# Optimization experiments

Hardware: AMD Instinct MI355X
Metric: run time of the kernel (lower is better)

## Reference

```python
import jax, jax.numpy as jnp
import numpy as np

B, N, DIM = 4, 2048, 1024
HEADS, DIM_HEAD = 16, 64
HIDDEN = HEADS * DIM_HEAD  # 1024
SCALE = 1.0 / np.sqrt(DIM_HEAD).astype(np.float32)


def setup_inputs() -> dict:
    key = jax.random.key(0)
    k1, k2, k3 = jax.random.split(key, 3)
    x = jax.random.normal(k1, (B, N, DIM), dtype=jnp.float32)
    # Linear(dim, 3*hidden, bias=False): stored as [in, out] for x @ W
    w_qkv = jax.random.normal(k2, (DIM, 3 * HIDDEN), dtype=jnp.float32) * (1.0 / np.sqrt(DIM))
    w_out = jax.random.normal(k3, (HIDDEN, DIM), dtype=jnp.float32) * (1.0 / np.sqrt(HIDDEN))
    b_out = jnp.zeros((DIM,), dtype=jnp.float32)
    return {"x": x, "w_qkv": w_qkv, "w_out": w_out, "b_out": b_out}


def reference(x, w_qkv, w_out, b_out):
    b, n, _ = x.shape
    qkv = x @ w_qkv                                  # [b, n, 3*hidden]
    q, k, v = jnp.split(qkv, 3, axis=-1)             # each [b, n, hidden]

    def to_heads(t):
        return t.reshape(b, n, HEADS, DIM_HEAD).transpose(0, 2, 1, 3)  # [b, h, n, d]

    q, k, v = to_heads(q), to_heads(k), to_heads(v)
    scores = jnp.einsum('bhid,bhjd->bhij', q, k) * SCALE   # [b, h, n_q, n_k]
    # Faithful to original: softmax over dim=2 (the QUERY axis), not keys.
    attn = jax.nn.softmax(scores, axis=2)
    y = jnp.einsum('bhij,bhjd->bhid', attn, v)             # [b, h, n, d]
    y = y.transpose(0, 2, 1, 3).reshape(b, n, HIDDEN)      # [b, n, hidden]
    return y @ w_out + b_out
```

## Files before the change

kernel.cpp:

```cpp
#include <hip/hip_runtime.h>
#include <math.h>
#include <stdint.h>

#define B_    4
#define N_    2048
#define DIM_  1024
#define H_    16
#define DH_   64
#define HID_  1024
#define RS_   3072
#define C2_   0.1803368801111204f

typedef unsigned short u16;
typedef unsigned int   u32;
typedef short  bf16x8 __attribute__((ext_vector_type(8)));
typedef u16    u16x8  __attribute__((ext_vector_type(8)));
typedef float  f32x4  __attribute__((ext_vector_type(4)));
typedef float  f32x16 __attribute__((ext_vector_type(16)));
typedef unsigned int u32x2 __attribute__((ext_vector_type(2)));

__device__ inline u16 f2b(float x) {
    u32 u = __float_as_uint(x);
    return (u16)((u + 0x7fffu + ((u >> 16) & 1u)) >> 16);
}
__device__ inline float b2f(u16 x) {
    return __uint_as_float((u32)x << 16);
}

__device__ inline u32 pack2bf(float f0, float f1) {
    u32 u0 = __float_as_uint(f0) + 0x8000u;
    u32 u1 = __float_as_uint(f1) + 0x8000u;
    return __builtin_amdgcn_perm(u1, u0, 0x07060302u);
}

__device__ inline void pl32swap(u32 &a, u32 &b) {
#if __has_builtin(__builtin_amdgcn_permlane32_swap)
    u32x2 r = __builtin_amdgcn_permlane32_swap(a, b, false, false);
    a = r[0]; b = r[1];
#else
    asm("v_permlane32_swap_b32 %0, %1" : "+v"(a), "+v"(b));
#endif
}

#if defined(__has_builtin)
#if __has_builtin(__builtin_amdgcn_global_load_lds)
#define USE_GLL 1
#endif
#endif

#ifdef USE_GLL
typedef const __attribute__((address_space(1))) u32* gas_ptr;
typedef __attribute__((address_space(3))) u32* las_ptr;
__device__ inline void gll16(const void* g, void* l) {
    __builtin_amdgcn_global_load_lds((gas_ptr)g, (las_ptr)l, 16, 0, 0);
}
#endif

__global__ __launch_bounds__(256) void cast_bf16(const float* __restrict__ in,
                                                 u16* __restrict__ out, int n) {
    int i = (blockIdx.x * 256 + threadIdx.x) * 8;
    if (i >= n) return;
    float4 a = *(const float4*)&in[i];
    float4 b = *(const float4*)&in[i + 4];
    u16x8 p;
    p[0] = f2b(a.x); p[1] = f2b(a.y); p[2] = f2b(a.z); p[3] = f2b(a.w);
    p[4] = f2b(b.x); p[5] = f2b(b.y); p[6] = f2b(b.z); p[7] = f2b(b.w);
    *(u16x8*)&out[i] = p;
}

__global__ __launch_bounds__(256) void transpose_cast(const float* __restrict__ W,
                                                      u16* __restrict__ Wt,
                                                      int K, int Nn, int qcols) {
    __shared__ float t[64][65];
    const int tid = threadIdx.x;
    const int k0 = blockIdx.y * 64, n0 = blockIdx.x * 64;
    for (int idx = tid; idx < 64 * 16; idx += 256) {
        int r = idx >> 4, c4 = (idx & 15) * 4;
        float4 g = *(const float4*)&W[(size_t)(k0 + r) * Nn + n0 + c4];
        t[r][c4] = g.x; t[r][c4 + 1] = g.y; t[r][c4 + 2] = g.z; t[r][c4 + 3] = g.w;
    }
    __syncthreads();
    for (int idx = tid; idx < 64 * 8; idx += 256) {
        int n = idx >> 3, k8 = (idx & 7) * 8;
        float s = (n0 + n < qcols) ? C2_ : 1.0f;
        u16x8 p;
        #pragma unroll
        for (int u = 0; u < 8; u++) p[u] = f2b(t[k8 + u][n] * s);
        *(u16x8*)&Wt[(size_t)(n0 + n) * K + k0 + k8] = p;
    }
}

template<int BF16OUT>
__global__ __launch_bounds__(256) void gemm_bt(const u16* __restrict__ A,
                                               const u16* __restrict__ Bt,
                                               const float* __restrict__ bias,
                                               void* __restrict__ Cout,
                                               int M, int Nn, int K) {
    __shared__ u16 at[128 * 32];
    __shared__ u16 bt[128 * 32];
    const int tid = threadIdx.x;
    const int lane = tid & 63, wave = tid >> 6;
    const int wr = wave >> 1, wc = wave & 1;
    const int mlane = lane & 15, quad = lane >> 4;
    const int id = blockIdx.x;
    const int mt = (id & 7) * 8 + ((id >> 3) & 7);
    const int nt = id >> 6;
    const int m0 = mt * 128, n0 = nt * 128;
    const int r = tid >> 2, kc = (tid & 3) * 8;

    f32x4 acc[4][4] = {};

    for (int k0 = 0; k0 < K; k0 += 32) {
        __syncthreads();
#ifdef USE_GLL
        gll16(&A[(size_t)(m0 + r) * K + k0 + kc],       &at[r * 32 + kc]);
        gll16(&A[(size_t)(m0 + r + 64) * K + k0 + kc],  &at[(r + 64) * 32 + kc]);
        gll16(&Bt[(size_t)(n0 + r) * K + k0 + kc],      &bt[r * 32 + kc]);
        gll16(&Bt[(size_t)(n0 + r + 64) * K + k0 + kc], &bt[(r + 64) * 32 + kc]);
#else
        *(u16x8*)&at[r * 32 + kc]        = *(const u16x8*)&A[(size_t)(m0 + r) * K + k0 + kc];
        *(u16x8*)&at[(r + 64) * 32 + kc] = *(const u16x8*)&A[(size_t)(m0 + r + 64) * K + k0 + kc];
        *(u16x8*)&bt[r * 32 + kc]        = *(const u16x8*)&Bt[(size_t)(n0 + r) * K + k0 + kc];
        *(u16x8*)&bt[(r + 64) * 32 + kc] = *(const u16x8*)&Bt[(size_t)(n0 + r + 64) * K + k0 + kc];
#endif
        __syncthreads();

        bf16x8 af[4], bf[4];
        #pragma unroll
        for (int rt = 0; rt < 4; rt++)
            af[rt] = *(const bf16x8*)&at[(wr * 64 + rt * 16 + mlane) * 32 + quad * 8];
        #pragma unroll
        for (int ct = 0; ct < 4; ct++)
            bf[ct] = *(const bf16x8*)&bt[(wc * 64 + ct * 16 + mlane) * 32 + quad * 8];
        #pragma unroll
        for (int rt = 0; rt < 4; rt++)
            #pragma unroll
            for (int ct = 0; ct < 4; ct++)
                acc[rt][ct] = __builtin_amdgcn_mfma_f32_16x16x32_bf16(af[rt], bf[ct], acc[rt][ct], 0, 0, 0);
    }

    const int row0 = m0 + wr * 64 + quad * 4;
    const int col0 = n0 + wc * 64 + mlane;
    #pragma unroll
    for (int rt = 0; rt < 4; rt++)
        #pragma unroll
        for (int ct = 0; ct < 4; ct++) {
            int c = col0 + ct * 16;
            float bv = (!BF16OUT && bias != nullptr) ? bias[c] : 0.f;
            #pragma unroll
            for (int reg = 0; reg < 4; reg++) {
                int rr = row0 + rt * 16 + reg;
                float v = acc[rt][ct][reg] + bv;
                if (BF16OUT) ((u16*)Cout)[(size_t)rr * Nn + c] = f2b(v);
                else         ((float*)Cout)[(size_t)rr * Nn + c] = v;
            }
        }
}

__global__ __launch_bounds__(256) void attn_stats_vt(const u16* __restrict__ qkvb,
                                                     u16* __restrict__ vT) {
    __shared__ u16 kt[64 * 72];
    __shared__ u16 qt[4][64 * 72];
    __shared__ float red[4][64];
    __shared__ float li[64];

    const int tid = threadIdx.x;
    const int lane = tid & 63, wave = tid >> 6;
    const int mlane = lane & 15, quad = lane >> 4;
    const int id = blockIdx.x;
    const int bh = (id & 7) * 8 + ((id >> 3) & 7);
    const int b = bh >> 4, h = bh & 15;
    const int j0 = (id >> 6) * 64;

    const u16* qbase = qkvb + (size_t)b * N_ * RS_ + h * DH_;
    const u16* kbase = qbase + HID_;
    const u16* vbase = qbase + 2 * HID_;

    for (int idx = tid; idx < 512; idx += 256) {
        int r = idx >> 3, d8 = (idx & 7) * 8;
        *(u16x8*)&kt[r * 72 + d8] = *(const u16x8*)&kbase[(size_t)(j0 + r) * RS_ + d8];
    }
    __syncthreads();

    bf16x8 kf[4][2];
    #pragma unroll
    for (int t = 0; t < 4; t++)
        #pragma unroll
        for (int ks = 0; ks < 2; ks++)
            kf[t][ks] = *(const bf16x8*)&kt[(t * 16 + mlane) * 72 + ks * 32 + quad * 8];

    f32x4 acc[4] = {};
    u16* qw = &qt[wave][0];

    const int prr = lane >> 3, pd8 = (lane & 7) * 8;
    u16x8 pq[8];
    #pragma unroll
    for (int t = 0; t < 8; t++)
        pq[t] = *(const u16x8*)&qbase[(size_t)(wave * 64 + t * 8 + prr) * RS_ + pd8];

    for (int i0 = wave * 64; i0 < N_; i0 += 256) {
        #pragma unroll
        for (int t = 0; t < 8; t++)
            *(u16x8*)&qw[(t * 8 + prr) * 72 + pd8] = pq[t];
        int in = i0 + 256;
        if (in < N_) {
            #pragma unroll
            for (int t = 0; t < 8; t++)
                pq[t] = *(const u16x8*)&qbase[(size_t)(in + t * 8 + prr) * RS_ + pd8];
        }
        #pragma unroll
        for (int q4 = 0; q4 < 4; q4++) {
            bf16x8 bq0 = *(const bf16x8*)&qw[(q4 * 16 + mlane) * 72 + quad * 8];
            bf16x8 bq1 = *(const bf16x8*)&qw[(q4 * 16 + mlane) * 72 + 32 + quad * 8];
            #pragma unroll
            for (int t = 0; t < 4; t++) {
                f32x4 z = {0.f, 0.f, 0.f, 0.f};
                z = __builtin_amdgcn_mfma_f32_16x16x32_bf16(kf[t][0], bq0, z, 0, 0, 0);
                z = __builtin_amdgcn_mfma_f32_16x16x32_bf16(kf[t][1], bq1, z, 0, 0, 0);
                #pragma unroll
                for (int reg = 0; reg < 4; reg++)
                    acc[t][reg] += __builtin_amdgcn_exp2f(z[reg]);
            }
        }
    }

    #pragma unroll
    for (int t = 0; t < 4; t++)
        #pragma unroll
        for (int reg = 0; reg < 4; reg++) {
            float v = acc[t][reg];
            v += __shfl_xor(v, 1, 64);
            v += __shfl_xor(v, 2, 64);
            v += __shfl_xor(v, 4, 64);
            v += __shfl_xor(v, 8, 64);
            if (mlane == 0) red[wave][t * 16 + quad * 4 + reg] = v;
        }
    __syncthreads();
    if (tid < 64) {
        float l = red[0][tid] + red[1][tid] + red[2][tid] + red[3][tid];
        li[tid] = 1.0f / l;
    }

    for (int idx = tid; idx < 512; idx += 256) {
        int r = idx >> 3, d8 = (idx & 7) * 8;
        *(u16x8*)&kt[r * 72 + d8] = *(const u16x8*)&vbase[(size_t)(j0 + r) * RS_ + d8];
    }
    __syncthreads();
    {
        int d = tid >> 2, j16 = (tid & 3) * 16;
        u16x8 p0, p1;
        #pragma unroll
        for (int u = 0; u < 8; u++) {
            p0[u] = f2b(b2f(kt[(j16 + u) * 72 + d]) * li[j16 + u]);
            p1[u] = f2b(b2f(kt[(j16 + 8 + u) * 72 + d]) * li[j16 + 8 + u]);
        }
        size_t o = ((size_t)bh * DH_ + d) * N_ + j0 + j16;
        *(u16x8*)&vT[o] = p0;
        *(u16x8*)&vT[o + 8] = p1;
    }
}

__global__ __launch_bounds__(256) void attn_apply(const u16* __restrict__ qkvb,
                                                  const u16* __restrict__ vT,
                                                  u16* __restrict__ yb) {
    __shared__ u16 S[256 * 72];

    const int tid = threadIdx.x;
    const int lane = tid & 63, wave = tid >> 6;
    const int m31 = lane & 31, half = lane >> 5;
    const int bh = blockIdx.y, b = bh >> 4, h = bh & 15;
    const int i0 = blockIdx.x * 256;

    const u16* qbase = qkvb + (size_t)b * N_ * RS_ + h * DH_;
    const u16* kbase = qbase + HID_;
    const u16* vbase = vT + (size_t)bh * DH_ * N_;

    for (int idx = tid; idx < 2048; idx += 256) {
        int r = idx >> 3, d8 = (idx & 7) * 8;
        *(u16x8*)&S[r * 72 + d8] = *(const u16x8*)&qbase[(size_t)(i0 + r) * RS_ + d8];
    }
    __syncthreads();

    bf16x8 qf[2][4];
    #pragma unroll
    for (int qc = 0; qc < 2; qc++)
        #pragma unroll
        for (int ks = 0; ks < 4; ks++)
            qf[qc][ks] = *(const bf16x8*)&S[(wave * 64 + qc * 32 + m31) * 72 + ks * 16 + half * 8];

    const int pr = tid >> 3, pc8 = (tid & 7) * 8;
    u16x8 pk0, pk1, pv0, pv1;
    pk0 = *(const u16x8*)&kbase[(size_t)pr * RS_ + pc8];
    pk1 = *(const u16x8*)&kbase[(size_t)(pr + 32) * RS_ + pc8];
    pv0 = *(const u16x8*)&vbase[(size_t)pr * N_ + pc8];
    pv1 = *(const u16x8*)&vbase[(size_t)(pr + 32) * N_ + pc8];

    f32x16 yacc[2][2] = {};

    for (int j0 = 0; j0 < N_; j0 += 64) {
        __syncthreads();
        *(u16x8*)&S[pr * 72 + pc8]        = pk0;
        *(u16x8*)&S[(pr + 32) * 72 + pc8] = pk1;
        *(u16x8*)&S[(pr + 64) * 72 + pc8] = pv0;
        *(u16x8*)&S[(pr + 96) * 72 + pc8] = pv1;
        __syncthreads();

        int jn = j0 + 64;
        if (jn < N_) {
            pk0 = *(const u16x8*)&kbase[(size_t)(jn + pr) * RS_ + pc8];
            pk1 = *(const u16x8*)&kbase[(size_t)(jn + pr + 32) * RS_ + pc8];
            pv0 = *(const u16x8*)&vbase[(size_t)pr * N_ + jn + pc8];
            pv1 = *(const u16x8*)&vbase[(size_t)(pr + 32) * N_ + jn + pc8];
        }

        bf16x8 pa[2][4];
        #pragma unroll
        for (int kt = 0; kt < 2; kt++) {
            bf16x8 ka[4];
            #pragma unroll
            for (int ks = 0; ks < 4; ks++)
                ka[ks] = *(const bf16x8*)&S[(kt * 32 + m31) * 72 + ks * 16 + half * 8];

            f32x16 sc[2] = {};
            #pragma unroll
            for (int ks = 0; ks < 4; ks++)
                #pragma unroll
                for (int qc = 0; qc < 2; qc++)
                    sc[qc] = __builtin_amdgcn_mfma_f32_32x32x16_bf16(ka[ks], qf[qc][ks], sc[qc], 0, 0, 0);

            #pragma unroll
            for (int qc = 0; qc < 2; qc++) {
                u32 P[4][2];
                #pragma unroll
                for (int rb = 0; rb < 4; rb++)
                    #pragma unroll
                    for (int pp = 0; pp < 2; pp++) {
                        float e0 = __builtin_amdgcn_exp2f(sc[qc][4 * rb + 2 * pp]);
                        float e1 = __builtin_amdgcn_exp2f(sc[qc][4 * rb + 2 * pp + 1]);
                        P[rb][pp] = pack2bf(e0, e1);
                    }
                #pragma unroll
                for (int ksl = 0; ksl < 2; ksl++) {
                    pl32swap(P[2 * ksl][0], P[2 * ksl + 1][0]);
                    pl32swap(P[2 * ksl][1], P[2 * ksl + 1][1]);
                    union { u32 u[4]; bf16x8 v; } cv;
                    cv.u[0] = P[2 * ksl][0];
                    cv.u[1] = P[2 * ksl][1];
                    cv.u[2] = P[2 * ksl + 1][0];
                    cv.u[3] = P[2 * ksl + 1][1];
                    pa[qc][2 * kt + ksl] = cv.v;
                }
            }
        }

        #pragma unroll
        for (int ks16 = 0; ks16 < 4; ks16++) {
            bf16x8 vb0 = *(const bf16x8*)&S[(64 + m31) * 72 + ks16 * 16 + half * 8];
            bf16x8 vb1 = *(const bf16x8*)&S[(96 + m31) * 72 + ks16 * 16 + half * 8];
            #pragma unroll
            for (int qc = 0; qc < 2; qc++) {
                yacc[qc][0] = __builtin_amdgcn_mfma_f32_32x32x16_bf16(pa[qc][ks16], vb0, yacc[qc][0], 0, 0, 0);
                yacc[qc][1] = __builtin_amdgcn_mfma_f32_32x32x16_bf16(pa[qc][ks16], vb1, yacc[qc][1], 0, 0, 0);
            }
        }
    }

    #pragma unroll
    for (int qc = 0; qc < 2; qc++)
        #pragma unroll
        for (int dt = 0; dt < 2; dt++)
            #pragma unroll
            for (int reg = 0; reg < 16; reg++) {
                int q = i0 + wave * 64 + qc * 32 + (reg & 3) + 8 * (reg >> 2) + 4 * half;
                yb[((size_t)b * N_ + q) * HID_ + h * DH_ + dt * 32 + m31] = f2b(yacc[qc][dt][reg]);
            }
}

extern "C" void kernel_launch(void* const* d_in, const int* in_sizes, int n_in,
                              void* d_out, int out_size, void* d_ws, size_t ws_size,
                              hipStream_t stream) {
    (void)in_sizes; (void)n_in; (void)out_size; (void)ws_size;

    const float* x     = (const float*)d_in[0];
    const float* w_qkv = (const float*)d_in[1];
    const float* w_out = (const float*)d_in[2];
    const float* b_out = (const float*)d_in[3];

    u16* xb    = (u16*)d_ws;
    u16* wqkvT = xb    + (size_t)8192 * 1024;
    u16* woutT = wqkvT + (size_t)3072 * 1024;
    u16* qkvb  = woutT + (size_t)1024 * 1024;
    u16* vTb   = qkvb  + (size_t)8192 * 3072;
    u16* yb    = vTb   + (size_t)64 * 64 * 2048;

    cast_bf16<<<4096, 256, 0, stream>>>(x, xb, 8192 * 1024);
    transpose_cast<<<dim3(3072 / 64, 1024 / 64), 256, 0, stream>>>(w_qkv, wqkvT, 1024, 3072, HID_);
    transpose_cast<<<dim3(1024 / 64, 1024 / 64), 256, 0, stream>>>(w_out, woutT, 1024, 1024, 0);

    gemm_bt<1><<<64 * 24, 256, 0, stream>>>(
        xb, wqkvT, nullptr, qkvb, 8192, 3072, 1024);

    attn_stats_vt<<<32 * 64, 256, 0, stream>>>(qkvb, vTb);

    attn_apply<<<dim3(N_ / 256, 64), 256, 0, stream>>>(qkvb, vTb, yb);

    gemm_bt<0><<<64 * 8, 256, 0, stream>>>(
        yb, woutT, b_out, d_out, 8192, 1024, 1024);
}
```

Before: 348.5 us.

## Halve attn_apply query tile to 128 rows and swizzle block order

Each attn_apply block now covers 128 query rows instead of 256, so every wave handles one 32-row query chunk. The grid doubles to 1024 one-dimensional blocks, and the block index is remapped so that consecutive blocks go to different (b,h) groups, which aims to spread K/V reads across XCDs or caches. The intent is more blocks and lower register pressure, which should raise occupancy and fill the 256 CUs better. The cost is that each K/V tile loaded into shared memory is now reused for half as many queries, so K/V global traffic doubles.

```diff
diff --git a/kernel.cpp b/kernel.cpp
--- a/kernel.cpp
+++ b/kernel.cpp
@@ -263,30 +263,30 @@
 __global__ __launch_bounds__(256) void attn_apply(const u16* __restrict__ qkvb,
                                                   const u16* __restrict__ vT,
                                                   u16* __restrict__ yb) {
-    __shared__ u16 S[256 * 72];
+    __shared__ u16 S[128 * 72];
 
     const int tid = threadIdx.x;
     const int lane = tid & 63, wave = tid >> 6;
     const int m31 = lane & 31, half = lane >> 5;
-    const int bh = blockIdx.y, b = bh >> 4, h = bh & 15;
-    const int i0 = blockIdx.x * 256;
+
+    const int v = (blockIdx.x & 7) * 128 + (blockIdx.x >> 3);
+    const int bh = v >> 4, b = bh >> 4, h = bh & 15;
+    const int i0 = (v & 15) * 128;
 
     const u16* qbase = qkvb + (size_t)b * N_ * RS_ + h * DH_;
     const u16* kbase = qbase + HID_;
     const u16* vbase = vT + (size_t)bh * DH_ * N_;
 
-    for (int idx = tid; idx < 2048; idx += 256) {
+    for (int idx = tid; idx < 1024; idx += 256) {
         int r = idx >> 3, d8 = (idx & 7) * 8;
         *(u16x8*)&S[r * 72 + d8] = *(const u16x8*)&qbase[(size_t)(i0 + r) * RS_ + d8];
     }
     __syncthreads();
 
-    bf16x8 qf[2][4];
-    #pragma unroll
-    for (int qc = 0; qc < 2; qc++)
-        #pragma unroll
-        for (int ks = 0; ks < 4; ks++)
-            qf[qc][ks] = *(const bf16x8*)&S[(wave * 64 + qc * 32 + m31) * 72 + ks * 16 + half * 8];
+    bf16x8 qf[4];
+    #pragma unroll
+    for (int ks = 0; ks < 4; ks++)
+        qf[ks] = *(const bf16x8*)&S[(wave * 32 + m31) * 72 + ks * 16 + half * 8];
 
     const int pr = tid >> 3, pc8 = (tid & 7) * 8;
     u16x8 pk0, pk1, pv0, pv1;
@@ -295,7 +295,7 @@
     pv0 = *(const u16x8*)&vbase[(size_t)pr * N_ + pc8];
     pv1 = *(const u16x8*)&vbase[(size_t)(pr + 32) * N_ + pc8];
 
-    f32x16 yacc[2][2] = {};
+    f32x16 yacc[2] = {};
 
     for (int j0 = 0; j0 < N_; j0 += 64) {
         __syncthreads();
@@ -313,7 +313,7 @@
             pv1 = *(const u16x8*)&vbase[(size_t)(pr + 32) * N_ + jn + pc8];
         }
 
-        bf16x8 pa[2][4];
+        bf16x8 pa[4];
         #pragma unroll
         for (int kt = 0; kt < 2; kt++) {
             bf16x8 ka[4];
@@ -321,35 +321,30 @@
             for (int ks = 0; ks < 4; ks++)
                 ka[ks] = *(const bf16x8*)&S[(kt * 32 + m31) * 72 + ks * 16 + half * 8];
 
-            f32x16 sc[2] = {};
+            f32x16 sc = {};
             #pragma unroll
             for (int ks = 0; ks < 4; ks++)
+                sc = __builtin_amdgcn_mfma_f32_32x32x16_bf16(ka[ks], qf[ks], sc, 0, 0, 0);
+
+            u32 P[4][2];
+            #pragma unroll
+            for (int rb = 0; rb < 4; rb++)
                 #pragma unroll
-                for (int qc = 0; qc < 2; qc++)
-                    sc[qc] = __builtin_amdgcn_mfma_f32_32x32x16_bf16(ka[ks], qf[qc][ks], sc[qc], 0, 0, 0);
-
-            #pragma unroll
-            for (int qc = 0; qc < 2; qc++) {
-                u32 P[4][2];
-                #pragma unroll
-                for (int rb = 0; rb < 4; rb++)
-                    #pragma unroll
-                    for (int pp = 0; pp < 2; pp++) {
-                        float e0 = __builtin_amdgcn_exp2f(sc[qc][4 * rb + 2 * pp]);
-                        float e1 = __builtin_amdgcn_exp2f(sc[qc][4 * rb + 2 * pp + 1]);
-                        P[rb][pp] = pack2bf(e0, e1);
-                    }
-                #pragma unroll
-                for (int ksl = 0; ksl < 2; ksl++) {
-                    pl32swap(P[2 * ksl][0], P[2 * ksl + 1][0]);
-                    pl32swap(P[2 * ksl][1], P[2 * ksl + 1][1]);
-                    union { u32 u[4]; bf16x8 v; } cv;
-                    cv.u[0] = P[2 * ksl][0];
-                    cv.u[1] = P[2 * ksl][1];
-                    cv.u[2] = P[2 * ksl + 1][0];
-                    cv.u[3] = P[2 * ksl + 1][1];
-                    pa[qc][2 * kt + ksl] = cv.v;
+                for (int pp = 0; pp < 2; pp++) {
+                    float e0 = __builtin_amdgcn_exp2f(sc[4 * rb + 2 * pp]);
+                    float e1 = __builtin_amdgcn_exp2f(sc[4 * rb + 2 * pp + 1]);
+                    P[rb][pp] = pack2bf(e0, e1);
                 }
+            #pragma unroll
+            for (int ksl = 0; ksl < 2; ksl++) {
+                pl32swap(P[2 * ksl][0], P[2 * ksl + 1][0]);
+                pl32swap(P[2 * ksl][1], P[2 * ksl + 1][1]);
+                union { u32 u[4]; bf16x8 v; } cv;
+                cv.u[0] = P[2 * ksl][0];
+                cv.u[1] = P[2 * ksl][1];
+                cv.u[2] = P[2 * ksl + 1][0];
+                cv.u[3] = P[2 * ksl + 1][1];
+                pa[2 * kt + ksl] = cv.v;
             }
         }
 
@@ -357,23 +352,18 @@
         for (int ks16 = 0; ks16 < 4; ks16++) {
             bf16x8 vb0 = *(const bf16x8*)&S[(64 + m31) * 72 + ks16 * 16 + half * 8];
             bf16x8 vb1 = *(const bf16x8*)&S[(96 + m31) * 72 + ks16 * 16 + half * 8];
-            #pragma unroll
-            for (int qc = 0; qc < 2; qc++) {
-                yacc[qc][0] = __builtin_amdgcn_mfma_f32_32x32x16_bf16(pa[qc][ks16], vb0, yacc[qc][0], 0, 0, 0);
-                yacc[qc][1] = __builtin_amdgcn_mfma_f32_32x32x16_bf16(pa[qc][ks16], vb1, yacc[qc][1], 0, 0, 0);
-            }
-        }
-    }
-
-    #pragma unroll
-    for (int qc = 0; qc < 2; qc++)
-        #pragma unroll
-        for (int dt = 0; dt < 2; dt++)
-            #pragma unroll
-            for (int reg = 0; reg < 16; reg++) {
-                int q = i0 + wave * 64 + qc * 32 + (reg & 3) + 8 * (reg >> 2) + 4 * half;
-                yb[((size_t)b * N_ + q) * HID_ + h * DH_ + dt * 32 + m31] = f2b(yacc[qc][dt][reg]);
-            }
+            yacc[0] = __builtin_amdgcn_mfma_f32_32x32x16_bf16(pa[ks16], vb0, yacc[0], 0, 0, 0);
+            yacc[1] = __builtin_amdgcn_mfma_f32_32x32x16_bf16(pa[ks16], vb1, yacc[1], 0, 0, 0);
+        }
+    }
+
+    #pragma unroll
+    for (int dt = 0; dt < 2; dt++)
+        #pragma unroll
+        for (int reg = 0; reg < 16; reg++) {
+            int q = i0 + wave * 32 + (reg & 3) + 8 * (reg >> 2) + 4 * half;
+            yb[((size_t)b * N_ + q) * HID_ + h * DH_ + dt * 32 + m31] = f2b(yacc[dt][reg]);
+        }
 }
 
 extern "C" void kernel_launch(void* const* d_in, const int* in_sizes, int n_in,
@@ -402,7 +392,7 @@
 
     attn_stats_vt<<<32 * 64, 256, 0, stream>>>(qkvb, vTb);
 
-    attn_apply<<<dim3(N_ / 256, 64), 256, 0, stream>>>(qkvb, vTb, yb);
+    attn_apply<<<1024, 256, 0, stream>>>(qkvb, vTb, yb);
 
     gemm_bt<0><<<64 * 8, 256, 0, stream>>>(
         yb, woutT, b_out, d_out, 8192, 1024, 1024);
```

New measurement: 343.5 us. No clear change (-1.5%).
